# Kernel optimization log

Measured on AMD Instinct MI355X. Metric: run time of the kernel, lower is better.

Reference implementation:

```python
import jax, jax.numpy as jnp
import numpy as np

MODEL_DIM = 1024
TOTAL_DIM = 1024
N_HEADS = 16
HEAD_DIM = TOTAL_DIM // N_HEADS


def setup_inputs() -> dict:
    key = jax.random.key(0)
    k1, k2, k3 = jax.random.split(key, 3)
    query = jax.random.normal(k1, (2, 2048, MODEL_DIM), dtype=jnp.float32)
    # nn.Linear(model_dim, 3*total_dim, bias=False): store as [in, out] for x @ W
    W_in = jax.random.normal(k2, (MODEL_DIM, 3 * TOTAL_DIM), dtype=jnp.float32) / np.sqrt(MODEL_DIM)
    W_out = jax.random.normal(k3, (TOTAL_DIM, MODEL_DIM), dtype=jnp.float32) / np.sqrt(TOTAL_DIM)
    return {"query": query, "W_in": W_in, "W_out": W_out}


def reference(query, W_in, W_out):
    B, S, _ = query.shape
    qkv = query @ W_in                      # [B, S, 3*D]
    q, k, v = jnp.split(qkv, 3, axis=-1)    # each [B, S, D]

    def to_heads(t):
        return t.reshape(B, S, N_HEADS, HEAD_DIM).transpose(0, 2, 1, 3)  # [B,H,S,d]

    q, k, v = to_heads(q), to_heads(k), to_heads(v)
    scale = 1.0 / np.sqrt(HEAD_DIM).astype(np.float32)
    scores = jnp.einsum('bhqd,bhkd->bhqk', q, k) * scale  # [B,H,S,S]
    causal = jnp.tril(jnp.ones((S, S), dtype=bool))
    scores = jnp.where(causal, scores, jnp.finfo(scores.dtype).min)
    probs = jax.nn.softmax(scores, axis=-1)
    attn = jnp.einsum('bhqk,bhkd->bhqd', probs, v)        # [B,H,S,d]
    attn = attn.transpose(0, 2, 1, 3).reshape(B, S, TOTAL_DIM)
    return attn @ W_out                     # [B, S, model_dim]
```

## Files before the change

### kernel.cpp

```cpp
#include <hip/hip_runtime.h>


typedef __bf16 bf16x8 __attribute__((ext_vector_type(8)));
typedef float f32x4 __attribute__((ext_vector_type(4)));
typedef int i32x4 __attribute__((ext_vector_type(4)));

#define B_   2
#define S_   2048
#define DM   1024
#define NH   16
#define HD   64
#define N3   3072
#define M_   4096

#define SCALE_LOG2E 0.180336884f

__device__ __forceinline__ unsigned short f2bf(float f) {
  unsigned int u = __float_as_uint(f);
  u += 0x7fffu + ((u >> 16) & 1u);
  return (unsigned short)(u >> 16);
}

__device__ __forceinline__ void gload_lds16(void* lds, const void* g) {
  __builtin_amdgcn_global_load_lds(
      (__attribute__((address_space(1))) void*)g,
      (__attribute__((address_space(3))) void*)lds, 16, 0, 0);
}

__global__ __launch_bounds__(256) void f32_to_bf16_vec(
    const float4* __restrict__ in, unsigned short* __restrict__ out, int n4) {
  int i = blockIdx.x * 256 + threadIdx.x;
  if (i < n4) {
    float4 v = in[i];
    ushort4 o;
    o.x = f2bf(v.x); o.y = f2bf(v.y); o.z = f2bf(v.z); o.w = f2bf(v.w);
    *(ushort4*)(&out[(size_t)i * 4]) = o;
  }
}

__global__ __launch_bounds__(256) void transpose_f32_bf16(
    const float* __restrict__ in, unsigned short* __restrict__ out, int R, int C) {
  __shared__ float tile[32][33];
  const int tx = threadIdx.x, ty = threadIdx.y;
  const int x = blockIdx.x * 32 + tx;
  const int y0 = blockIdx.y * 32;
#pragma unroll
  for (int j = 0; j < 32; j += 8)
    tile[ty + j][tx] = in[(size_t)(y0 + ty + j) * C + x];
  __syncthreads();
  const int ox = y0 + tx;
  const int oy0 = blockIdx.x * 32;
#pragma unroll
  for (int j = 0; j < 32; j += 8)
    out[(size_t)(oy0 + ty + j) * R + ox] = f2bf(tile[tx][ty + j]);
}

__global__ __launch_bounds__(256) void transpose_v(
    const unsigned short* __restrict__ qkv, unsigned short* __restrict__ vT) {
  __shared__ unsigned short tile[32][33];
  const int tx = threadIdx.x, ty = threadIdx.y;
  const int c0 = blockIdx.x * 32;
  const int r0 = blockIdx.y * 32;
#pragma unroll
  for (int j = 0; j < 32; j += 8)
    tile[ty + j][tx] = qkv[(size_t)(r0 + ty + j) * N3 + 2 * DM + c0 + tx];
  __syncthreads();
  const int b = r0 >> 11;
  const int srow = (r0 & 2047);
  const int head = c0 >> 6;
#pragma unroll
  for (int j = 0; j < 32; j += 8) {
    const int d = (c0 & 63) + ty + j;
    vT[(size_t)((b * NH + head) * HD + d) * S_ + srow + tx] = tile[tx][ty + j];
  }
}

template <int OUT_BF16>
__global__ __launch_bounds__(256) void gemm_abt(
    const unsigned short* __restrict__ A, const unsigned short* __restrict__ Bt,
    void* __restrict__ Cv, int M, int N, int K) {
  __shared__ __align__(16) unsigned short a_sm[128 * 32];
  __shared__ __align__(16) unsigned short b_sm[128 * 32];
  const int tid = threadIdx.x;
  const int lane = tid & 63, wave = tid >> 6;
  const int quad = lane >> 4, l15 = lane & 15;
  const int row0 = blockIdx.y * 128, col0 = blockIdx.x * 128;
  const int wm = (wave >> 1) * 64, wn = (wave & 1) * 64;

  f32x4 acc[4][4];
#pragma unroll
  for (int i = 0; i < 4; i++)
#pragma unroll
    for (int j = 0; j < 4; j++) acc[i][j] = (f32x4){0.f, 0.f, 0.f, 0.f};

  const int e0 = tid * 8;

  for (int k0 = 0; k0 < K; k0 += 32) {
    __syncthreads();
#pragma unroll
    for (int i = 0; i < 2; i++) {
      int e = e0 + i * 2048;
      int r = e >> 5, c = e & 31;
      gload_lds16(&a_sm[e], &A[(size_t)(row0 + r) * K + k0 + c]);
      gload_lds16(&b_sm[e], &Bt[(size_t)(col0 + r) * K + k0 + c]);
    }
    __syncthreads();

    bf16x8 af[4], bfb[4];
#pragma unroll
    for (int i = 0; i < 4; i++) {
      af[i]  = *(const bf16x8*)&a_sm[(wm + i * 16 + l15) * 32 + quad * 8];
      bfb[i] = *(const bf16x8*)&b_sm[(wn + i * 16 + l15) * 32 + quad * 8];
    }
#pragma unroll
    for (int i = 0; i < 4; i++)
#pragma unroll
      for (int j = 0; j < 4; j++)
        acc[i][j] = __builtin_amdgcn_mfma_f32_16x16x32_bf16(af[i], bfb[j], acc[i][j], 0, 0, 0);
  }

#pragma unroll
  for (int i = 0; i < 4; i++) {
#pragma unroll
    for (int j = 0; j < 4; j++) {
#pragma unroll
      for (int r = 0; r < 4; r++) {
        const int row = row0 + wm + i * 16 + quad * 4 + r;
        const int col = col0 + wn + j * 16 + l15;
        const float v = acc[i][j][r];
        if (OUT_BF16)
          ((unsigned short*)Cv)[(size_t)row * N + col] = f2bf(v);
        else
          ((float*)Cv)[(size_t)row * N + col] = v;
      }
    }
  }
}

__global__ __launch_bounds__(512, 4) void attn_fused4(
    const unsigned short* __restrict__ qkv,
    const unsigned short* __restrict__ vT,
    unsigned short* __restrict__ attnout) {
  const int h = blockIdx.y, b = blockIdx.z;
  const int j = blockIdx.x;
  const int tid = threadIdx.x;
  const int lane = tid & 63, wave = tid >> 6;
  const int quad = lane >> 4, l15 = lane & 15;
  const int sw = l15 & 7;

  __shared__ __align__(16) unsigned short k_sm[2 * 4096];
  __shared__ __align__(16) unsigned short vt_sm[2 * 4096];

  const int wrow0 = (wave < 4) ? (j * 64 + wave * 16)
                               : ((31 - j) * 64 + (wave - 4) * 16);
  const int qrow = wrow0 + l15;

  bf16x8 qf[2];
  {
    const unsigned short* qp = qkv + (size_t)(b * S_ + qrow) * N3 + h * HD + quad * 8;
    qf[0] = *(const bf16x8*)qp;
    qf[1] = *(const bf16x8*)(qp + 32);
  }

  f32x4 o[4];
#pragma unroll
  for (int n = 0; n < 4; n++) o[n] = (f32x4){0.f, 0.f, 0.f, 0.f};
  float lsum = 0.f;

  const int r0s = tid >> 3;
  const int gch = ((tid & 7) ^ (r0s & 7)) * 8;
  const unsigned short* kgb = qkv + (size_t)(b * S_ + r0s) * N3 + DM + h * HD + gch;
  const unsigned short* vgb = vT + (size_t)((b * NH + h) * HD + r0s) * S_ + gch;

  const int addrA = (((quad * 2) & 3) * 16 + l15) * 4;
  const int addrB = (((quad * 2 + 1) & 3) * 16 + l15) * 4;

  const int nt = 32 - j;
  gload_lds16(&k_sm[tid * 8], kgb);
  gload_lds16(&vt_sm[tid * 8], vgb);

  for (int t = 0; t < nt; t++) {
    __syncthreads();
    if (t + 1 < nt) {
      const int nb = ((t + 1) & 1) * 4096;
      gload_lds16(&k_sm[nb + tid * 8], kgb + (size_t)(t + 1) * 64 * N3);
      gload_lds16(&vt_sm[nb + tid * 8], vgb + (t + 1) * 64);
    }
    if (t * 64 > wrow0 + 15) continue;

    const unsigned short* kb = &k_sm[(t & 1) * 4096];
    const unsigned short* vb = &vt_sm[(t & 1) * 4096];

    f32x4 s[4];
#pragma unroll
    for (int mb = 0; mb < 4; mb++) s[mb] = (f32x4){0.f, 0.f, 0.f, 0.f};
#pragma unroll
    for (int mb = 0; mb < 4; mb++) {
      const int ro = (mb * 16 + l15) * 64;
      bf16x8 kf0 = *(const bf16x8*)&kb[ro + ((quad ^ sw) << 3)];
      bf16x8 kf1 = *(const bf16x8*)&kb[ro + (((4 + quad) ^ sw) << 3)];
      s[mb] = __builtin_amdgcn_mfma_f32_16x16x32_bf16(kf0, qf[0], s[mb], 0, 0, 0);
      s[mb] = __builtin_amdgcn_mfma_f32_16x16x32_bf16(kf1, qf[1], s[mb], 0, 0, 0);
    }

    if (t * 64 + 63 <= wrow0) {
#pragma unroll
      for (int mb = 0; mb < 4; mb++)
#pragma unroll
        for (int r = 0; r < 4; r++)
          s[mb][r] = exp2f(s[mb][r] * SCALE_LOG2E);
    } else {
      const int kb0 = t * 64 + quad * 4;
#pragma unroll
      for (int mb = 0; mb < 4; mb++)
#pragma unroll
        for (int r = 0; r < 4; r++) {
          const float e = exp2f(s[mb][r] * SCALE_LOG2E);
          s[mb][r] = (kb0 + mb * 16 + r <= qrow) ? e : 0.f;
        }
    }
#pragma unroll
    for (int mb = 0; mb < 4; mb++)
      lsum += (s[mb][0] + s[mb][1]) + (s[mb][2] + s[mb][3]);

    int pk[4][2];
#pragma unroll
    for (int mb = 0; mb < 4; mb++) {
      const unsigned u0 = __float_as_uint(s[mb][0]) + 0x8000u;
      const unsigned u1 = __float_as_uint(s[mb][1]) + 0x8000u;
      const unsigned u2 = __float_as_uint(s[mb][2]) + 0x8000u;
      const unsigned u3 = __float_as_uint(s[mb][3]) + 0x8000u;
      pk[mb][0] = (int)__builtin_amdgcn_perm(u1, u0, 0x07060302u);
      pk[mb][1] = (int)__builtin_amdgcn_perm(u3, u2, 0x07060302u);
    }

    const bool hi = quad >= 2;
#pragma unroll
    for (int ks = 0; ks < 2; ks++) {
      const int m0 = 2 * ks, m1 = m0 + 1;
      const int f0a = __builtin_amdgcn_ds_bpermute(addrA, pk[m0][0]);
      const int f0b = __builtin_amdgcn_ds_bpermute(addrA, pk[m1][0]);
      const int f1a = __builtin_amdgcn_ds_bpermute(addrA, pk[m0][1]);
      const int f1b = __builtin_amdgcn_ds_bpermute(addrA, pk[m1][1]);
      const int f2a = __builtin_amdgcn_ds_bpermute(addrB, pk[m0][0]);
      const int f2b = __builtin_amdgcn_ds_bpermute(addrB, pk[m1][0]);
      const int f3a = __builtin_amdgcn_ds_bpermute(addrB, pk[m0][1]);
      const int f3b = __builtin_amdgcn_ds_bpermute(addrB, pk[m1][1]);
      i32x4 fr;
      fr.x = hi ? f0b : f0a;
      fr.y = hi ? f1b : f1a;
      fr.z = hi ? f2b : f2a;
      fr.w = hi ? f3b : f3a;
      const bf16x8 pfrag = __builtin_bit_cast(bf16x8, fr);
#pragma unroll
      for (int mb = 0; mb < 4; mb++) {
        const int ro = (mb * 16 + l15) * 64;
        bf16x8 vf = *(const bf16x8*)&vb[ro + (((ks * 4 + quad) ^ sw) << 3)];
        o[mb] = __builtin_amdgcn_mfma_f32_16x16x32_bf16(vf, pfrag, o[mb], 0, 0, 0);
      }
    }
  }

  float l = lsum;
  l += __shfl_xor(l, 16);
  l += __shfl_xor(l, 32);
  const float inv = 1.0f / l;
  const size_t grow = (size_t)(b * S_ + qrow);
#pragma unroll
  for (int mb = 0; mb < 4; mb++) {
    ushort4 w;
    w.x = f2bf(o[mb][0] * inv);
    w.y = f2bf(o[mb][1] * inv);
    w.z = f2bf(o[mb][2] * inv);
    w.w = f2bf(o[mb][3] * inv);
    *(ushort4*)&attnout[grow * DM + h * HD + mb * 16 + quad * 4] = w;
  }
}

extern "C" void kernel_launch(void* const* d_in, const int* in_sizes, int n_in,
                              void* d_out, int out_size, void* d_ws, size_t ws_size,
                              hipStream_t stream) {
  const float* query = (const float*)d_in[0];
  const float* w_in  = (const float*)d_in[1];
  const float* w_out = (const float*)d_in[2];
  float* out = (float*)d_out;

  char* ws = (char*)d_ws;
  unsigned short* qbf     = (unsigned short*)(ws);
  unsigned short* vT      = (unsigned short*)(ws);
  unsigned short* w_in_t  = (unsigned short*)(ws + 8388608);
  unsigned short* w_out_t = (unsigned short*)(ws + 14680064);
  unsigned short* qkv     = (unsigned short*)(ws + 16777216);
  unsigned short* attn    = (unsigned short*)(ws + 41943040);

  f32_to_bf16_vec<<<dim3(M_ * DM / 1024), dim3(256), 0, stream>>>(
      (const float4*)query, qbf, M_ * DM / 4);
  transpose_f32_bf16<<<dim3(N3 / 32, DM / 32), dim3(32, 8), 0, stream>>>(w_in, w_in_t, DM, N3);
  transpose_f32_bf16<<<dim3(DM / 32, DM / 32), dim3(32, 8), 0, stream>>>(w_out, w_out_t, DM, DM);
  gemm_abt<1><<<dim3(N3 / 128, M_ / 128), dim3(256), 0, stream>>>(qbf, w_in_t, qkv, M_, N3, DM);
  transpose_v<<<dim3(DM / 32, M_ / 32), dim3(32, 8), 0, stream>>>(qkv, vT);
  attn_fused4<<<dim3(16, NH, B_), dim3(512), 0, stream>>>(qkv, vT, attn);
  gemm_abt<0><<<dim3(DM / 128, M_ / 128), dim3(256), 0, stream>>>(attn, w_out_t, out, M_, DM, DM);
}
```

Before: 206.2 us.

## Split attention into 256-thread blocks and fold softmax scale into W_in

The attention kernel drops from 512 to 256 threads per block and doubles the grid. Each block now pairs two 32-row query groups from opposite ends of the causal triangle to balance work, and each thread issues two K/V tile loads per stage. The softmax scale times log2e is pre-multiplied into the Q columns of the transposed W_in, which removes a multiply per score inside the attention loop. The risk is that each small block reloads K/V tiles that were previously shared by eight waves, and bf16 rounding of the scaled Q weights shifts numerics slightly.

```diff
diff --git a/kernel.cpp b/kernel.cpp
--- a/kernel.cpp
+++ b/kernel.cpp
@@ -39,7 +39,8 @@
 }
 
 __global__ __launch_bounds__(256) void transpose_f32_bf16(
-    const float* __restrict__ in, unsigned short* __restrict__ out, int R, int C) {
+    const float* __restrict__ in, unsigned short* __restrict__ out, int R, int C,
+    int scale_rows, float scale) {
   __shared__ float tile[32][33];
   const int tx = threadIdx.x, ty = threadIdx.y;
   const int x = blockIdx.x * 32 + tx;
@@ -51,8 +52,12 @@
   const int ox = y0 + tx;
   const int oy0 = blockIdx.x * 32;
 #pragma unroll
-  for (int j = 0; j < 32; j += 8)
-    out[(size_t)(oy0 + ty + j) * R + ox] = f2bf(tile[tx][ty + j]);
+  for (int j = 0; j < 32; j += 8) {
+    const int orow = oy0 + ty + j;
+    float v = tile[tx][ty + j];
+    if (orow < scale_rows) v *= scale;
+    out[(size_t)orow * R + ox] = f2bf(v);
+  }
 }
 
 __global__ __launch_bounds__(256) void transpose_v(
@@ -137,7 +142,7 @@
   }
 }
 
-__global__ __launch_bounds__(512, 4) void attn_fused4(
+__global__ __launch_bounds__(256, 4) void attn_fused6(
     const unsigned short* __restrict__ qkv,
     const unsigned short* __restrict__ vT,
     unsigned short* __restrict__ attnout) {
@@ -151,8 +156,8 @@
   __shared__ __align__(16) unsigned short k_sm[2 * 4096];
   __shared__ __align__(16) unsigned short vt_sm[2 * 4096];
 
-  const int wrow0 = (wave < 4) ? (j * 64 + wave * 16)
-                               : ((31 - j) * 64 + (wave - 4) * 16);
+  const int grp = (wave < 2) ? j : (63 - j);
+  const int wrow0 = grp * 32 + (wave & 1) * 16;
   const int qrow = wrow0 + l15;
 
   bf16x8 qf[2];
@@ -175,16 +180,23 @@
   const int addrA = (((quad * 2) & 3) * 16 + l15) * 4;
   const int addrB = (((quad * 2 + 1) & 3) * 16 + l15) * 4;
 
-  const int nt = 32 - j;
+  const int nt = (((63 - j) * 32 + 31) >> 6) + 1;
+
   gload_lds16(&k_sm[tid * 8], kgb);
+  gload_lds16(&k_sm[tid * 8 + 2048], kgb + (size_t)32 * N3);
   gload_lds16(&vt_sm[tid * 8], vgb);
+  gload_lds16(&vt_sm[tid * 8 + 2048], vgb + (size_t)32 * S_);
 
   for (int t = 0; t < nt; t++) {
     __syncthreads();
     if (t + 1 < nt) {
       const int nb = ((t + 1) & 1) * 4096;
-      gload_lds16(&k_sm[nb + tid * 8], kgb + (size_t)(t + 1) * 64 * N3);
-      gload_lds16(&vt_sm[nb + tid * 8], vgb + (t + 1) * 64);
+      const unsigned short* kgt = kgb + (size_t)(t + 1) * 64 * N3;
+      const unsigned short* vgt = vgb + (t + 1) * 64;
+      gload_lds16(&k_sm[nb + tid * 8], kgt);
+      gload_lds16(&k_sm[nb + tid * 8 + 2048], kgt + (size_t)32 * N3);
+      gload_lds16(&vt_sm[nb + tid * 8], vgt);
+      gload_lds16(&vt_sm[nb + tid * 8 + 2048], vgt + (size_t)32 * S_);
     }
     if (t * 64 > wrow0 + 15) continue;
 
@@ -208,15 +220,15 @@
       for (int mb = 0; mb < 4; mb++)
 #pragma unroll
         for (int r = 0; r < 4; r++)
-          s[mb][r] = exp2f(s[mb][r] * SCALE_LOG2E);
+          s[mb][r] = exp2f(s[mb][r]);
     } else {
-      const int kb0 = t * 64 + quad * 4;
+      const int kq0 = t * 64 + quad * 4;
 #pragma unroll
       for (int mb = 0; mb < 4; mb++)
 #pragma unroll
         for (int r = 0; r < 4; r++) {
-          const float e = exp2f(s[mb][r] * SCALE_LOG2E);
-          s[mb][r] = (kb0 + mb * 16 + r <= qrow) ? e : 0.f;
+          const float e = exp2f(s[mb][r]);
+          s[mb][r] = (kq0 + mb * 16 + r <= qrow) ? e : 0.f;
         }
     }
 #pragma unroll
@@ -295,10 +307,12 @@
 
   f32_to_bf16_vec<<<dim3(M_ * DM / 1024), dim3(256), 0, stream>>>(
       (const float4*)query, qbf, M_ * DM / 4);
-  transpose_f32_bf16<<<dim3(N3 / 32, DM / 32), dim3(32, 8), 0, stream>>>(w_in, w_in_t, DM, N3);
-  transpose_f32_bf16<<<dim3(DM / 32, DM / 32), dim3(32, 8), 0, stream>>>(w_out, w_out_t, DM, DM);
+  transpose_f32_bf16<<<dim3(N3 / 32, DM / 32), dim3(32, 8), 0, stream>>>(
+      w_in, w_in_t, DM, N3, DM, SCALE_LOG2E);
+  transpose_f32_bf16<<<dim3(DM / 32, DM / 32), dim3(32, 8), 0, stream>>>(
+      w_out, w_out_t, DM, DM, 0, 1.0f);
   gemm_abt<1><<<dim3(N3 / 128, M_ / 128), dim3(256), 0, stream>>>(qbf, w_in_t, qkv, M_, N3, DM);
   transpose_v<<<dim3(DM / 32, M_ / 32), dim3(32, 8), 0, stream>>>(qkv, vT);
-  attn_fused4<<<dim3(16, NH, B_), dim3(512), 0, stream>>>(qkv, vT, attn);
+  attn_fused6<<<dim3(32, NH, B_), dim3(256), 0, stream>>>(qkv, vT, attn);
   gemm_abt<0><<<dim3(DM / 128, M_ / 128), dim3(256), 0, stream>>>(attn, w_out_t, out, M_, DM, DM);
 }
```

Result: no change. 206.5 us (+0.1%).
